# Performance work log

Measured on AMD Instinct MI355X. Metric: run time of the kernel, lower is better.

The kernel has to match this reference:

```python
import jax, jax.numpy as jnp
import numpy as np

NEG_MASK = -987654321.0  # constant used by the original module for the diagonal self-mask


def setup_inputs() -> dict:
    key = jax.random.key(0)
    kq, kk, kv = jax.random.split(key, 3)
    B, L, S, H, E, D = 8, 1024, 1024, 12, 64, 64
    queries = jax.random.normal(kq, (B, L, H, E), dtype=jnp.float32)
    keys = jax.random.normal(kk, (B, S, H, E), dtype=jnp.float32)
    values = jax.random.normal(kv, (B, S, H, D), dtype=jnp.float32)
    # LSA per-head learnable scale, initialized to (1/sqrt(E)) * ones(H)
    scale = jnp.full((H,), 1.0 / np.sqrt(E), dtype=jnp.float32)
    return {"queries": queries, "keys": keys, "values": values, "scale": scale}


def reference(queries, keys, values, scale):
    # queries: [B,L,H,E], keys: [B,S,H,E], values: [B,S,H,D], scale: [H]
    B, L, H, E = queries.shape
    S = keys.shape[1]
    # scores: [B,H,L,S] with per-head scale
    scores = jnp.einsum('blhe,bshe->bhls', queries, keys) * scale[None, :, None, None]
    # diagonal self-mask (LSA): set scores[b,h,i,i] = NEG_MASK
    eye = jnp.eye(L, S, dtype=bool)
    scores = jnp.where(eye[None, None, :, :], NEG_MASK, scores)
    A = jax.nn.softmax(scores, axis=-1)  # dropout is identity in eval mode
    V = jnp.einsum('bhls,bshd->blhd', A, values)
    return V, A
```

## Files before the change

kernel.cpp:

```cpp
#include <hip/hip_runtime.h>

#define B_ 8
#define L_ 1024
#define S_ 1024
#define H_ 12
#define E_ 64
#define D_ 64

#define TL 32
#define TS 64
#define NT 512
#define NITER (S_ / TS)

#define QW (E_ + 8)
#define KW (E_ + 8)
#define VW (TS + 8)
#define PW (S_ + 8)

typedef short bf8 __attribute__((ext_vector_type(8)));
typedef float f32x4 __attribute__((ext_vector_type(4)));

__device__ __forceinline__ unsigned short f2bf(float f) {
  unsigned int u = __builtin_bit_cast(unsigned int, f);
  u += 0x7fffu + ((u >> 16) & 1u);
  return (unsigned short)(u >> 16);
}
__device__ __forceinline__ float bf2f(unsigned short us) {
  unsigned int u = ((unsigned int)us) << 16;
  return __builtin_bit_cast(float, u);
}

__global__ __launch_bounds__(NT, 1) void attn_fused(
    const float* __restrict__ Q, const float* __restrict__ K,
    const float* __restrict__ V, const float* __restrict__ SC,
    float* __restrict__ OUTV, float* __restrict__ OUTA)
{
  __shared__ __align__(16) unsigned short Qs[TL * QW];
  __shared__ __align__(16) unsigned short Ks[TS * KW];
  __shared__ __align__(16) unsigned short Vt[D_ * VW];
  __shared__ __align__(16) unsigned short P[TL * PW];
  __shared__ float rowsum[TL];
  __shared__ float rinv[TL];

  const int t = threadIdx.x;

  const int blk = blockIdx.x;
  const int x   = blk & 7;
  const int j   = blk >> 3;
  const int bh  = x * 12 + (j >> 5);
  const int lt  = j & 31;
  const int b   = bh / H_;
  const int h   = bh - b * H_;
  const int l0  = lt * TL;

  const float scale_h = SC[h];

  const int w    = t >> 6;
  const int lane = t & 63;
  const int quad = lane >> 4;
  const int l16  = lane & 15;
  const int rowblk  = w & 1;
  const int colblk  = w >> 1;
  const int rowbase = rowblk * 16;

  if (t < TL) rowsum[t] = 0.0f;

  {
    const int r = t >> 4;
    const int c = (t & 15) * 4;
    const float4 q4 = *reinterpret_cast<const float4*>(
        Q + (((size_t)(b * L_ + l0 + r) * H_ + h) * E_ + c));
    unsigned short* dst = &Qs[r * QW + c];
    dst[0] = f2bf(q4.x); dst[1] = f2bf(q4.y);
    dst[2] = f2bf(q4.z); dst[3] = f2bf(q4.w);
  }

  float psum[4] = {0.f, 0.f, 0.f, 0.f};
  const int krow = t >> 3;
  const int kcol = (t & 7) * 8;

  for (int it = 0; it < NITER; ++it) {
    __syncthreads();
    {
      const int s = it * TS + krow;
      const float* src = K + (((size_t)(b * S_ + s) * H_ + h) * E_ + kcol);
      const float4 a0 = *reinterpret_cast<const float4*>(src);
      const float4 a1 = *reinterpret_cast<const float4*>(src + 4);
      unsigned short* dst = &Ks[krow * KW + kcol];
      dst[0] = f2bf(a0.x); dst[1] = f2bf(a0.y);
      dst[2] = f2bf(a0.z); dst[3] = f2bf(a0.w);
      dst[4] = f2bf(a1.x); dst[5] = f2bf(a1.y);
      dst[6] = f2bf(a1.z); dst[7] = f2bf(a1.w);
    }
    __syncthreads();

    f32x4 sacc = {0.f, 0.f, 0.f, 0.f};
    {
      const bf8 a0 = *(const bf8*)&Qs[(rowbase + l16) * QW + 0  + quad * 8];
      const bf8 b0 = *(const bf8*)&Ks[(colblk * 16 + l16) * KW + 0  + quad * 8];
      sacc = __builtin_amdgcn_mfma_f32_16x16x32_bf16(a0, b0, sacc, 0, 0, 0);
      const bf8 a1 = *(const bf8*)&Qs[(rowbase + l16) * QW + 32 + quad * 8];
      const bf8 b1 = *(const bf8*)&Ks[(colblk * 16 + l16) * KW + 32 + quad * 8];
      sacc = __builtin_amdgcn_mfma_f32_16x16x32_bf16(a1, b1, sacc, 0, 0, 0);
    }

    const int sg = it * TS + colblk * 16 + l16;
#pragma unroll
    for (int r = 0; r < 4; ++r) {
      const int lrow = rowbase + quad * 4 + r;
      const int lg = l0 + lrow;
      float p = __expf(sacc[r] * scale_h);
      if (sg == lg) p = 0.f;
      P[lrow * PW + it * TS + colblk * 16 + l16] = f2bf(p);
      psum[r] += p;
    }
  }

#pragma unroll
  for (int r = 0; r < 4; ++r) {
    float v = psum[r];
    v += __shfl_xor(v, 8, 16);
    v += __shfl_xor(v, 4, 16);
    v += __shfl_xor(v, 2, 16);
    v += __shfl_xor(v, 1, 16);
    if (l16 == 0) atomicAdd(&rowsum[rowbase + quad * 4 + r], v);
  }
  __syncthreads();
  if (t < TL) rinv[t] = 1.0f / rowsum[t];
  __syncthreads();

  {
    const size_t abase = (((size_t)(b * H_ + h)) * L_ + l0) * S_;
#pragma unroll
    for (int itw = 0; itw < 16; ++itw) {
      const int flat4 = itw * NT + t;
      const int row = flat4 >> 8;
      const int c4  = flat4 & 255;
      const unsigned short* ps = &P[row * PW + c4 * 4];
      const float ri = rinv[row];
      float4 o;
      o.x = bf2f(ps[0]) * ri;
      o.y = bf2f(ps[1]) * ri;
      o.z = bf2f(ps[2]) * ri;
      o.w = bf2f(ps[3]) * ri;
      *reinterpret_cast<float4*>(OUTA + abase + (size_t)row * S_ + c4 * 4) = o;
    }
  }

  f32x4 oacc = {0.f, 0.f, 0.f, 0.f};
  const int vrow = t >> 3;
  const int vcol = (t & 7) * 8;

  for (int it = 0; it < NITER; ++it) {
    __syncthreads();
    {
      const int s = it * TS + vrow;
      const float* src = V + (((size_t)(b * S_ + s) * H_ + h) * D_ + vcol);
      const float4 a0 = *reinterpret_cast<const float4*>(src);
      const float4 a1 = *reinterpret_cast<const float4*>(src + 4);
      Vt[(vcol + 0) * VW + vrow] = f2bf(a0.x);
      Vt[(vcol + 1) * VW + vrow] = f2bf(a0.y);
      Vt[(vcol + 2) * VW + vrow] = f2bf(a0.z);
      Vt[(vcol + 3) * VW + vrow] = f2bf(a0.w);
      Vt[(vcol + 4) * VW + vrow] = f2bf(a1.x);
      Vt[(vcol + 5) * VW + vrow] = f2bf(a1.y);
      Vt[(vcol + 6) * VW + vrow] = f2bf(a1.z);
      Vt[(vcol + 7) * VW + vrow] = f2bf(a1.w);
    }
    __syncthreads();

    const bf8 pa0 = *(const bf8*)&P[(rowbase + l16) * PW + it * TS + 0  + quad * 8];
    const bf8 vb0 = *(const bf8*)&Vt[(colblk * 16 + l16) * VW + 0  + quad * 8];
    oacc = __builtin_amdgcn_mfma_f32_16x16x32_bf16(pa0, vb0, oacc, 0, 0, 0);
    const bf8 pa1 = *(const bf8*)&P[(rowbase + l16) * PW + it * TS + 32 + quad * 8];
    const bf8 vb1 = *(const bf8*)&Vt[(colblk * 16 + l16) * VW + 32 + quad * 8];
    oacc = __builtin_amdgcn_mfma_f32_16x16x32_bf16(pa1, vb1, oacc, 0, 0, 0);
  }

#pragma unroll
  for (int r = 0; r < 4; ++r) {
    const int lrow = rowbase + quad * 4 + r;
    const int lg = l0 + lrow;
    const float ri = rinv[lrow];
    OUTV[(((size_t)(b * L_ + lg)) * H_ + h) * D_ + colblk * 16 + l16] =
        oacc[r] * ri;
  }
}

extern "C" void kernel_launch(void* const* d_in, const int* in_sizes, int n_in,
                              void* d_out, int out_size, void* d_ws, size_t ws_size,
                              hipStream_t stream) {
  (void)in_sizes; (void)n_in; (void)out_size; (void)d_ws; (void)ws_size;
  const float* Q  = (const float*)d_in[0];
  const float* K  = (const float*)d_in[1];
  const float* V  = (const float*)d_in[2];
  const float* SC = (const float*)d_in[3];
  float* OUTV = (float*)d_out;
  float* OUTA = OUTV + (size_t)B_ * L_ * H_ * D_;

  const dim3 grid(B_ * H_ * (L_ / TL));
  attn_fused<<<grid, NT, 0, stream>>>(Q, K, V, SC, OUTV, OUTA);
}
```

Measured before the change: 877.5 us.

## Split key range across waves with per-wave P tiles and LDS reduction of outputs

Each of the eight waves now owns a 128-key slice and computes both QK^T and PV for all 32 query rows. K and V fragments load straight from global into registers, so the shared K/V staging and the per-iteration block barriers go away. Unnormalized probabilities stay packed in registers and are written to the attention output after the row sums are known. Partial outputs are combined with LDS atomics. This also drops the large full-row P buffer, so the launch bound is raised to allow more blocks per CU. The cost is uncoalesced strided global reads of V per element and a heavy register footprint from the packed probabilities.

```diff
diff --git a/kernel.cpp b/kernel.cpp
--- a/kernel.cpp
+++ b/kernel.cpp
@@ -8,37 +8,34 @@
 #define D_ 64
 
 #define TL 32
-#define TS 64
 #define NT 512
-#define NITER (S_ / TS)
-
-#define QW (E_ + 8)
-#define KW (E_ + 8)
-#define VW (TS + 8)
-#define PW (S_ + 8)
+#define NSUB 4
+
+#define QW 72
+#define PSW 40
+#define OBW 68
 
 typedef short bf8 __attribute__((ext_vector_type(8)));
 typedef float f32x4 __attribute__((ext_vector_type(4)));
 
-__device__ __forceinline__ unsigned short f2bf(float f) {
+static __device__ __forceinline__ unsigned short f2bf(float f) {
   unsigned int u = __builtin_bit_cast(unsigned int, f);
   u += 0x7fffu + ((u >> 16) & 1u);
   return (unsigned short)(u >> 16);
 }
-__device__ __forceinline__ float bf2f(unsigned short us) {
+static __device__ __forceinline__ float bf2f(unsigned short us) {
   unsigned int u = ((unsigned int)us) << 16;
   return __builtin_bit_cast(float, u);
 }
 
-__global__ __launch_bounds__(NT, 1) void attn_fused(
+__global__ __launch_bounds__(NT, 4) void attn_fused(
     const float* __restrict__ Q, const float* __restrict__ K,
     const float* __restrict__ V, const float* __restrict__ SC,
     float* __restrict__ OUTV, float* __restrict__ OUTA)
 {
   __shared__ __align__(16) unsigned short Qs[TL * QW];
-  __shared__ __align__(16) unsigned short Ks[TS * KW];
-  __shared__ __align__(16) unsigned short Vt[D_ * VW];
-  __shared__ __align__(16) unsigned short P[TL * PW];
+  __shared__ __align__(16) unsigned short Psub[8][32 * PSW];
+  __shared__ __align__(16) float Obuf[TL * OBW];
   __shared__ float rowsum[TL];
   __shared__ float rinv[TL];
 
@@ -46,9 +43,9 @@
 
   const int blk = blockIdx.x;
   const int x   = blk & 7;
-  const int j   = blk >> 3;
-  const int bh  = x * 12 + (j >> 5);
-  const int lt  = j & 31;
+  const int jj_ = blk >> 3;
+  const int bh  = x * 12 + (jj_ >> 5);
+  const int lt  = jj_ & 31;
   const int b   = bh / H_;
   const int h   = bh - b * H_;
   const int l0  = lt * TL;
@@ -57,12 +54,11 @@
 
   const int w    = t >> 6;
   const int lane = t & 63;
-  const int quad = lane >> 4;
-  const int l16  = lane & 15;
-  const int rowblk  = w & 1;
-  const int colblk  = w >> 1;
-  const int rowbase = rowblk * 16;
-
+  const int g    = lane >> 4;
+  const int c16  = lane & 15;
+  const int sw   = w * 128;
+
+  for (int i = t; i < TL * OBW; i += NT) Obuf[i] = 0.0f;
   if (t < TL) rowsum[t] = 0.0f;
 
   {
@@ -74,116 +70,168 @@
     dst[0] = f2bf(q4.x); dst[1] = f2bf(q4.y);
     dst[2] = f2bf(q4.z); dst[3] = f2bf(q4.w);
   }
-
-  float psum[4] = {0.f, 0.f, 0.f, 0.f};
-  const int krow = t >> 3;
-  const int kcol = (t & 7) * 8;
-
-  for (int it = 0; it < NITER; ++it) {
-    __syncthreads();
-    {
-      const int s = it * TS + krow;
-      const float* src = K + (((size_t)(b * S_ + s) * H_ + h) * E_ + kcol);
-      const float4 a0 = *reinterpret_cast<const float4*>(src);
-      const float4 a1 = *reinterpret_cast<const float4*>(src + 4);
-      unsigned short* dst = &Ks[krow * KW + kcol];
-      dst[0] = f2bf(a0.x); dst[1] = f2bf(a0.y);
-      dst[2] = f2bf(a0.z); dst[3] = f2bf(a0.w);
-      dst[4] = f2bf(a1.x); dst[5] = f2bf(a1.y);
-      dst[6] = f2bf(a1.z); dst[7] = f2bf(a1.w);
+  __syncthreads();
+
+  const size_t kbase = ((size_t)b * S_ * H_ + h) * (size_t)E_;
+  const size_t vbase = ((size_t)b * S_ * H_ + h) * (size_t)D_;
+
+  float psum[2][4] = {{0.f,0.f,0.f,0.f},{0.f,0.f,0.f,0.f}};
+  f32x4 oacc[2][4];
+#pragma unroll
+  for (int m = 0; m < 2; ++m)
+#pragma unroll
+    for (int n = 0; n < 4; ++n) oacc[m][n] = (f32x4){0.f,0.f,0.f,0.f};
+
+  unsigned int pp[NSUB][2][2][2];
+
+  unsigned short* Pw = &Psub[w][0];
+
+#pragma unroll
+  for (int sub = 0; sub < NSUB; ++sub) {
+    const int s0 = sw + sub * 32;
+
+    bf8 kf[2][2];
+#pragma unroll
+    for (int n = 0; n < 2; ++n)
+#pragma unroll
+      for (int ks = 0; ks < 2; ++ks) {
+        const float* src =
+            K + kbase + (size_t)(s0 + n * 16 + c16) * (H_ * E_) + ks * 32 + g * 8;
+        const float4 a0 = *reinterpret_cast<const float4*>(src);
+        const float4 a1 = *reinterpret_cast<const float4*>(src + 4);
+        bf8 kk;
+        kk[0] = (short)f2bf(a0.x); kk[1] = (short)f2bf(a0.y);
+        kk[2] = (short)f2bf(a0.z); kk[3] = (short)f2bf(a0.w);
+        kk[4] = (short)f2bf(a1.x); kk[5] = (short)f2bf(a1.y);
+        kk[6] = (short)f2bf(a1.z); kk[7] = (short)f2bf(a1.w);
+        kf[n][ks] = kk;
+      }
+
+    bf8 qf[2][2];
+#pragma unroll
+    for (int m = 0; m < 2; ++m)
+#pragma unroll
+      for (int ks = 0; ks < 2; ++ks)
+        qf[m][ks] = *reinterpret_cast<const bf8*>(
+            &Qs[(m * 16 + c16) * QW + ks * 32 + g * 8]);
+
+    f32x4 sacc[2][2];
+#pragma unroll
+    for (int m = 0; m < 2; ++m)
+#pragma unroll
+      for (int n = 0; n < 2; ++n) sacc[m][n] = (f32x4){0.f,0.f,0.f,0.f};
+#pragma unroll
+    for (int m = 0; m < 2; ++m)
+#pragma unroll
+      for (int n = 0; n < 2; ++n)
+#pragma unroll
+        for (int ks = 0; ks < 2; ++ks)
+          sacc[m][n] = __builtin_amdgcn_mfma_f32_16x16x32_bf16(
+              qf[m][ks], kf[n][ks], sacc[m][n], 0, 0, 0);
+
+#pragma unroll
+    for (int m = 0; m < 2; ++m)
+#pragma unroll
+      for (int n = 0; n < 2; ++n) {
+        unsigned int pk0 = 0, pk1 = 0;
+#pragma unroll
+        for (int r = 0; r < 4; ++r) {
+          const int lrow = m * 16 + g * 4 + r;
+          const int scol = s0 + n * 16 + c16;
+          float p = __expf(sacc[m][n][r] * scale_h);
+          if (scol == l0 + lrow) p = 0.0f;
+          psum[m][r] += p;
+          const unsigned int pb = f2bf(p);
+          if (r == 0) pk0 = pb;
+          else if (r == 1) pk0 |= pb << 16;
+          else if (r == 2) pk1 = pb;
+          else pk1 |= pb << 16;
+          Pw[lrow * PSW + n * 16 + c16] = (unsigned short)pb;
+        }
+        pp[sub][m][n][0] = pk0;
+        pp[sub][m][n][1] = pk1;
+      }
+
+    bf8 paf[2];
+#pragma unroll
+    for (int m = 0; m < 2; ++m)
+      paf[m] = *reinterpret_cast<const bf8*>(&Pw[(m * 16 + c16) * PSW + g * 8]);
+
+#pragma unroll
+    for (int n = 0; n < 4; ++n) {
+      const float* vsrc =
+          V + vbase + (size_t)(s0 + g * 8) * (H_ * D_) + n * 16 + c16;
+      bf8 vb;
+#pragma unroll
+      for (int j = 0; j < 8; ++j)
+        vb[j] = (short)f2bf(vsrc[(size_t)j * (H_ * D_)]);
+#pragma unroll
+      for (int m = 0; m < 2; ++m)
+        oacc[m][n] = __builtin_amdgcn_mfma_f32_16x16x32_bf16(
+            paf[m], vb, oacc[m][n], 0, 0, 0);
     }
-    __syncthreads();
-
-    f32x4 sacc = {0.f, 0.f, 0.f, 0.f};
-    {
-      const bf8 a0 = *(const bf8*)&Qs[(rowbase + l16) * QW + 0  + quad * 8];
-      const bf8 b0 = *(const bf8*)&Ks[(colblk * 16 + l16) * KW + 0  + quad * 8];
-      sacc = __builtin_amdgcn_mfma_f32_16x16x32_bf16(a0, b0, sacc, 0, 0, 0);
-      const bf8 a1 = *(const bf8*)&Qs[(rowbase + l16) * QW + 32 + quad * 8];
-      const bf8 b1 = *(const bf8*)&Ks[(colblk * 16 + l16) * KW + 32 + quad * 8];
-      sacc = __builtin_amdgcn_mfma_f32_16x16x32_bf16(a1, b1, sacc, 0, 0, 0);
+  }
+
+#pragma unroll
+  for (int m = 0; m < 2; ++m)
+#pragma unroll
+    for (int n = 0; n < 4; ++n)
+#pragma unroll
+      for (int r = 0; r < 4; ++r)
+        atomicAdd(&Obuf[(m * 16 + g * 4 + r) * OBW + n * 16 + c16],
+                  oacc[m][n][r]);
+
+#pragma unroll
+  for (int m = 0; m < 2; ++m)
+#pragma unroll
+    for (int r = 0; r < 4; ++r) {
+      float v = psum[m][r];
+      v += __shfl_xor(v, 8, 16);
+      v += __shfl_xor(v, 4, 16);
+      v += __shfl_xor(v, 2, 16);
+      v += __shfl_xor(v, 1, 16);
+      if (c16 == 0) atomicAdd(&rowsum[m * 16 + g * 4 + r], v);
     }
-
-    const int sg = it * TS + colblk * 16 + l16;
-#pragma unroll
-    for (int r = 0; r < 4; ++r) {
-      const int lrow = rowbase + quad * 4 + r;
-      const int lg = l0 + lrow;
-      float p = __expf(sacc[r] * scale_h);
-      if (sg == lg) p = 0.f;
-      P[lrow * PW + it * TS + colblk * 16 + l16] = f2bf(p);
-      psum[r] += p;
-    }
-  }
-
-#pragma unroll
-  for (int r = 0; r < 4; ++r) {
-    float v = psum[r];
-    v += __shfl_xor(v, 8, 16);
-    v += __shfl_xor(v, 4, 16);
-    v += __shfl_xor(v, 2, 16);
-    v += __shfl_xor(v, 1, 16);
-    if (l16 == 0) atomicAdd(&rowsum[rowbase + quad * 4 + r], v);
-  }
   __syncthreads();
   if (t < TL) rinv[t] = 1.0f / rowsum[t];
   __syncthreads();
 
   {
     const size_t abase = (((size_t)(b * H_ + h)) * L_ + l0) * S_;
-#pragma unroll
-    for (int itw = 0; itw < 16; ++itw) {
-      const int flat4 = itw * NT + t;
-      const int row = flat4 >> 8;
-      const int c4  = flat4 & 255;
-      const unsigned short* ps = &P[row * PW + c4 * 4];
-      const float ri = rinv[row];
-      float4 o;
-      o.x = bf2f(ps[0]) * ri;
-      o.y = bf2f(ps[1]) * ri;
-      o.z = bf2f(ps[2]) * ri;
-      o.w = bf2f(ps[3]) * ri;
-      *reinterpret_cast<float4*>(OUTA + abase + (size_t)row * S_ + c4 * 4) = o;
-    }
-  }
-
-  f32x4 oacc = {0.f, 0.f, 0.f, 0.f};
-  const int vrow = t >> 3;
-  const int vcol = (t & 7) * 8;
-
-  for (int it = 0; it < NITER; ++it) {
-    __syncthreads();
-    {
-      const int s = it * TS + vrow;
-      const float* src = V + (((size_t)(b * S_ + s) * H_ + h) * D_ + vcol);
-      const float4 a0 = *reinterpret_cast<const float4*>(src);
-      const float4 a1 = *reinterpret_cast<const float4*>(src + 4);
-      Vt[(vcol + 0) * VW + vrow] = f2bf(a0.x);
-      Vt[(vcol + 1) * VW + vrow] = f2bf(a0.y);
-      Vt[(vcol + 2) * VW + vrow] = f2bf(a0.z);
-      Vt[(vcol + 3) * VW + vrow] = f2bf(a0.w);
-      Vt[(vcol + 4) * VW + vrow] = f2bf(a1.x);
-      Vt[(vcol + 5) * VW + vrow] = f2bf(a1.y);
-      Vt[(vcol + 6) * VW + vrow] = f2bf(a1.z);
-      Vt[(vcol + 7) * VW + vrow] = f2bf(a1.w);
-    }
-    __syncthreads();
-
-    const bf8 pa0 = *(const bf8*)&P[(rowbase + l16) * PW + it * TS + 0  + quad * 8];
-    const bf8 vb0 = *(const bf8*)&Vt[(colblk * 16 + l16) * VW + 0  + quad * 8];
-    oacc = __builtin_amdgcn_mfma_f32_16x16x32_bf16(pa0, vb0, oacc, 0, 0, 0);
-    const bf8 pa1 = *(const bf8*)&P[(rowbase + l16) * PW + it * TS + 32 + quad * 8];
-    const bf8 vb1 = *(const bf8*)&Vt[(colblk * 16 + l16) * VW + 32 + quad * 8];
-    oacc = __builtin_amdgcn_mfma_f32_16x16x32_bf16(pa1, vb1, oacc, 0, 0, 0);
-  }
-
-#pragma unroll
-  for (int r = 0; r < 4; ++r) {
-    const int lrow = rowbase + quad * 4 + r;
-    const int lg = l0 + lrow;
-    const float ri = rinv[lrow];
-    OUTV[(((size_t)(b * L_ + lg)) * H_ + h) * D_ + colblk * 16 + l16] =
-        oacc[r] * ri;
+    float rv[2][4];
+#pragma unroll
+    for (int m = 0; m < 2; ++m)
+#pragma unroll
+      for (int r = 0; r < 4; ++r) rv[m][r] = rinv[m * 16 + g * 4 + r];
+#pragma unroll
+    for (int sub = 0; sub < NSUB; ++sub)
+#pragma unroll
+      for (int m = 0; m < 2; ++m)
+#pragma unroll
+        for (int n = 0; n < 2; ++n)
+#pragma unroll
+          for (int k = 0; k < 2; ++k) {
+            const unsigned int pk = pp[sub][m][n][k];
+            const int r0 = k * 2, r1 = k * 2 + 1;
+            const size_t col = (size_t)(sw + sub * 32 + n * 16 + c16);
+            OUTA[abase + (size_t)(m * 16 + g * 4 + r0) * S_ + col] =
+                bf2f((unsigned short)(pk & 0xffffu)) * rv[m][r0];
+            OUTA[abase + (size_t)(m * 16 + g * 4 + r1) * S_ + col] =
+                bf2f((unsigned short)(pk >> 16)) * rv[m][r1];
+          }
+  }
+
+  {
+    const int r = t >> 4;
+    const int d = (t & 15) * 4;
+    const float ri = rinv[r];
+    float4 o;
+    o.x = Obuf[r * OBW + d + 0] * ri;
+    o.y = Obuf[r * OBW + d + 1] * ri;
+    o.z = Obuf[r * OBW + d + 2] * ri;
+    o.w = Obuf[r * OBW + d + 3] * ri;
+    *reinterpret_cast<float4*>(
+        OUTV + (((size_t)(b * L_ + l0 + r)) * H_ + h) * D_ + d) = o;
   }
 }
 
```

Measured after the change: 1.098 ms. +25.1%, slower.
